# Performance work log

Measured on AMD Instinct MI355X. Metric: run time of the kernel, lower is better.

## Reference

```python
import jax, jax.numpy as jnp
import numpy as np

B, L, C, H, W = 1, 16, 32, 64, 64
HID = C // 2


def setup_inputs() -> dict:
    key = jax.random.key(0)
    ks = jax.random.split(key, 6)
    flows = jax.random.normal(ks[0], (B, L, 2, H, W), jnp.float32) * 0.05
    images = jax.random.normal(ks[1], (B, L, C, H, W), jnp.float32)
    w1 = jax.random.normal(ks[2], (HID, 2 * C), jnp.float32) * 0.05
    b1 = jax.random.normal(ks[3], (HID,), jnp.float32) * 0.05
    w2 = jax.random.normal(ks[4], (2, HID), jnp.float32) * 0.05
    b2 = jax.random.normal(ks[5], (2,), jnp.float32) * 0.01
    decay_log = jnp.asarray(-2.0, jnp.float32)
    return dict(flows=flows, images=images, decay_log=decay_log,
                w1=w1, b1=b1, w2=w2, b2=b2)


def _bilinear_sample(img, grid):
    # img: [C,H,W]; grid: [H,W,2] with (x,y) in [-1,1]; matches torch
    # grid_sample(mode='bilinear', padding_mode='zeros', align_corners=False)
    Cv, Hv, Wv = img.shape
    gx, gy = grid[..., 0], grid[..., 1]
    ix = ((gx + 1.0) * Wv - 1.0) * 0.5
    iy = ((gy + 1.0) * Hv - 1.0) * 0.5
    ix0 = jnp.floor(ix)
    iy0 = jnp.floor(iy)
    ix1, iy1 = ix0 + 1.0, iy0 + 1.0
    wx1 = ix - ix0
    wy1 = iy - iy0
    wx0 = 1.0 - wx1
    wy0 = 1.0 - wy1

    def corner(xi, yi, w):
        valid = (xi >= 0) & (xi < Wv) & (yi >= 0) & (yi < Hv)
        xc = jnp.clip(xi, 0, Wv - 1).astype(jnp.int32)
        yc = jnp.clip(yi, 0, Hv - 1).astype(jnp.int32)
        v = img[:, yc, xc]  # [C,H,W]
        return v * (w * valid.astype(img.dtype))[None]

    return (corner(ix0, iy0, wx0 * wy0) + corner(ix1, iy0, wx1 * wy0) +
            corner(ix0, iy1, wx0 * wy1) + corner(ix1, iy1, wx1 * wy1))


def _forward(flows, images, decay_log, w1, b1, w2, b2):
    Bv, Lv, Cv, Hv, Wv = images.shape
    cum = jnp.cumsum(flows, axis=1)                      # [B,L,2,H,W]
    rel = cum[:, :, None] - cum[:, None, :]              # [B,Lt,Lk,2,H,W]
    # residual 1x1 conv stack on concat(img_t, img_k)
    img_t = jnp.broadcast_to(images[:, :, None], (Bv, Lv, Lv, Cv, Hv, Wv))
    img_k = jnp.broadcast_to(images[:, None, :], (Bv, Lv, Lv, Cv, Hv, Wv))
    feat = jnp.concatenate([img_t, img_k], axis=3)       # [B,Lt,Lk,2C,H,W]
    h = jax.nn.relu(jnp.einsum('btkchw,oc->btkohw', feat, w1)
                    + b1[None, None, None, :, None, None])
    res = (jnp.einsum('btkohw,po->btkphw', h, w2)
           + b2[None, None, None, :, None, None])        # [B,Lt,Lk,2,H,W]
    rel = rel + res
    # base grid: pixel centers in [-1,1] (align_corners=False convention)
    gy = jnp.linspace(-1.0 + 1.0 / Hv, 1.0 - 1.0 / Hv, Hv, dtype=images.dtype)
    gx = jnp.linspace(-1.0 + 1.0 / Wv, 1.0 - 1.0 / Wv, Wv, dtype=images.dtype)
    base = jnp.stack(jnp.meshgrid(gx, gy, indexing='xy'), axis=-1)  # [H,W,2]
    grid = base + jnp.moveaxis(rel, 3, -1)               # [B,Lt,Lk,H,W,2]
    wrapped_x = jnp.mod(grid[..., 0] + 1.0, 2.0) - 1.0   # wrap x into [-1,1)
    grid = jnp.stack([wrapped_x, grid[..., 1]], axis=-1)
    # sample images[b,k] at grid[b,t,k] for all (t,k) pairs
    samp = jax.vmap(                                      # over batch
        jax.vmap(                                         # over t (grid only)
            jax.vmap(_bilinear_sample, (0, 0)),           # over k
            (None, 0)),
        (0, 0))(images, grid)                             # [B,Lt,Lk,C,H,W]
    # causal decay weights: exp(-exp(decay_log)*(t-k)) for k<=t, else 0
    tk = jnp.arange(Lv)[:, None] - jnp.arange(Lv)[None, :]
    wts = jnp.where(tk >= 0,
                    jnp.exp(-jnp.exp(decay_log) * tk.astype(images.dtype)),
                    jnp.zeros((), images.dtype))
    return jnp.einsum('btkchw,tk->btchw', samp, wts)


def reference(flows, images, decay_log, w1, b1, w2, b2):
    return _forward(flows, images, decay_log, w1, b1, w2, b2)
```

## Files before the change

kernel.cpp:

```cpp
#include <hip/hip_runtime.h>

#define LL 16
#define CC 32
#define HIDN 16
#define HH 64
#define WW 64
#define HW 4096
#define NCHUNK 40

#define CUM_OFF  0
#define U_OFF    (LL * 2 * HW)
#define V_OFF    (U_OFF + LL * HIDN * HW)
#define IMGC_OFF (V_OFF + LL * HIDN * HW)
#define A_OFF    (IMGC_OFF + LL * CC * HW / 2)

__device__ const int T_SORT[NCHUNK] = {
    0,1,2,3,4,5,6,7,8,9,10,11,12,13,14,15,
    4,5,6,7,8,9,10,11,12,13,14,15,
    8,9,10,11,12,13,14,15,
    12,13,14,15 };
__device__ const int KC_SORT[NCHUNK] = {
    0,0,0,0,0,0,0,0,0,0,0,0,0,0,0,0,
    1,1,1,1,1,1,1,1,1,1,1,1,
    2,2,2,2,2,2,2,2,
    3,3,3,3 };
__device__ const int SEG[4]  = {0, 16, 28, 36};
__device__ const int TMIN[4] = {0, 4, 8, 12};

__device__ inline unsigned short f2bf(float f) {
    unsigned u = __float_as_uint(f);
    unsigned r = (u + 0x7fffu + ((u >> 16) & 1u)) >> 16;
    return (unsigned short)r;
}
__device__ inline float bflo(unsigned u) { return __uint_as_float(u << 16); }
__device__ inline float bfhi(unsigned u) { return __uint_as_float(u & 0xffff0000u); }

__global__ __launch_bounds__(256) void cumsum_kernel(const float* __restrict__ flows,
                                                     float* __restrict__ cum) {
    int idx = blockIdx.x * 256 + threadIdx.x;
    float acc = 0.0f;
#pragma unroll
    for (int l = 0; l < LL; ++l) {
        acc += flows[l * 2 * HW + idx];
        cum[l * 2 * HW + idx] = acc;
    }
}

__global__ __launch_bounds__(256) void prep_kernel(const float* __restrict__ images,
                                                   const float* __restrict__ w1,
                                                   const float* __restrict__ b1,
                                                   float* __restrict__ ws) {
    __shared__ float w1s[HIDN * 2 * CC];
    const int tid = threadIdx.x;
    ((float4*)w1s)[tid] = ((const float4*)w1)[tid];
    __syncthreads();

    const int l  = blockIdx.y;
    const int px = blockIdx.x * 256 + tid;
    const float* img = images + (size_t)l * CC * HW;

    float x[CC];
#pragma unroll
    for (int c = 0; c < CC; ++c) x[c] = img[c * HW + px];

    float u[HIDN], v[HIDN];
#pragma unroll
    for (int o = 0; o < HIDN; ++o) { u[o] = 0.0f; v[o] = b1[o]; }
#pragma unroll
    for (int c = 0; c < CC; ++c) {
#pragma unroll
        for (int o = 0; o < HIDN; ++o) {
            u[o] = fmaf(w1s[o * 64 + c],      x[c], u[o]);
            v[o] = fmaf(w1s[o * 64 + CC + c], x[c], v[o]);
        }
    }

    float* Up = ws + U_OFF + (size_t)l * HIDN * HW + px;
    float* Vp = ws + V_OFF + (size_t)l * HIDN * HW + px;
#pragma unroll
    for (int o = 0; o < HIDN; ++o) {
        Up[o * HW] = u[o];
        Vp[o * HW] = v[o];
    }

    uint4* img4 = (uint4*)(ws + IMGC_OFF);
#pragma unroll
    for (int cg = 0; cg < 4; ++cg) {
        const int c0 = cg * 8;
        unsigned d[4];
#pragma unroll
        for (int q = 0; q < 4; ++q)
            d[q] = (unsigned)f2bf(x[c0 + 2 * q]) | ((unsigned)f2bf(x[c0 + 2 * q + 1]) << 16);
        img4[((size_t)(l * 4 + cg)) * HW + px] = make_uint4(d[0], d[1], d[2], d[3]);
    }
}

__global__ __launch_bounds__(256, 2) void sample_kernel(const float* __restrict__ ws_in,
                                                        float* __restrict__ ws_out,
                                                        const float* __restrict__ w2,
                                                        const float* __restrict__ b2,
                                                        const float* __restrict__ decay_log) {
    __shared__ float  w2s[2 * HIDN];
    __shared__ float  b2s2[2];
    __shared__ float2 dls[4][64];

    const int tid = threadIdx.x;
    if (tid < 2 * HIDN) w2s[tid] = w2[tid];
    if (tid < 2)        b2s2[tid] = b2[tid];
    __syncthreads();

    const int hwb = blockIdx.x;
    const int s   = (hwb & 7) * 320 + (hwb >> 3);
    const int cid = s >> 6;
    const int strip = s & 63;
    const int t   = T_SORT[cid];
    const int k0  = KC_SORT[cid] * 4;

    const float* cum = ws_in + CUM_OFF;
    const float* Ub  = ws_in + U_OFF;
    const float* Vb  = ws_in + V_OFF;
    const uint4* img4 = (const uint4*)(ws_in + IMGC_OFF);

    {
        const int kk  = tid >> 6;
        const int lp  = tid & 63;
        const int px1 = strip * 64 + lp;
        const int k1  = k0 + kk;

        const float* up = Ub + (size_t)t  * HIDN * HW + px1;
        const float* vp = Vb + (size_t)k1 * HIDN * HW + px1;

        float res0 = b2s2[0], res1 = b2s2[1];
#pragma unroll
        for (int o = 0; o < HIDN; ++o) {
            float h = fmaxf(up[o * HW] + vp[o * HW], 0.0f);
            res0 = fmaf(w2s[o],        h, res0);
            res1 = fmaf(w2s[HIDN + o], h, res1);
        }

        float dx = (cum[(t * 2)     * HW + px1] - cum[(k1 * 2)     * HW + px1]) + res0;
        float dy = (cum[(t * 2 + 1) * HW + px1] - cum[(k1 * 2 + 1) * HW + px1]) + res1;
        dls[kk][lp] = make_float2(dx, dy);
    }
    __syncthreads();

    const int lane = tid & 63;
    const int cg   = tid >> 6;
    const int px   = strip * 64 + lane;

    const float lam = expf(decay_log[0]);
    const float bgx = (float)(2 * lane  + 1) * (1.0f / 64.0f) - 1.0f;
    const float bgy = (float)(2 * strip + 1) * (1.0f / 64.0f) - 1.0f;

    int   off[4][4];
    float cwt[4][4];
#pragma unroll
    for (int dk = 0; dk < 4; ++dk) {
        const int k = k0 + dk;
        const float wtd = (k <= t) ? expf(-lam * (float)(t - k)) : 0.0f;
        float2 d = dls[dk][lane];

        float gx = bgx + d.x;
        float gy = bgy + d.y;

        float xp = gx + 1.0f;
        xp = xp - floorf(xp * 0.5f) * 2.0f;
        float gxw = xp - 1.0f;

        float ix = ((gxw + 1.0f) * 64.0f - 1.0f) * 0.5f;
        float iy = ((gy  + 1.0f) * 64.0f - 1.0f) * 0.5f;

        float ix0f = floorf(ix), iy0f = floorf(iy);
        float fx1 = ix - ix0f, fy1 = iy - iy0f;
        float fx0 = 1.0f - fx1, fy0 = 1.0f - fy1;
        int ix0 = (int)ix0f, iy0 = (int)iy0f;
        int ix1 = ix0 + 1,   iy1 = iy0 + 1;

        int xi[4] = {ix0, ix1, ix0, ix1};
        int yi[4] = {iy0, iy0, iy1, iy1};
        float wwv[4] = {fx0 * fy0, fx1 * fy0, fx0 * fy1, fx1 * fy1};
#pragma unroll
        for (int j = 0; j < 4; ++j) {
            bool valid = (xi[j] >= 0) & (xi[j] < WW) & (yi[j] >= 0) & (yi[j] < HH);
            int xc = min(max(xi[j], 0), WW - 1);
            int yc = min(max(yi[j], 0), HH - 1);
            off[dk][j] = yc * WW + xc;
            cwt[dk][j] = valid ? wwv[j] * wtd : 0.0f;
        }
    }

    uint4 q[4][4];
#pragma unroll
    for (int dk = 0; dk < 4; ++dk) {
        const size_t pb = (size_t)((k0 + dk) * 4 + cg) * HW;
#pragma unroll
        for (int j = 0; j < 4; ++j)
            q[dk][j] = img4[pb + off[dk][j]];
    }

    float acc[8];
#pragma unroll
    for (int j = 0; j < 8; ++j) acc[j] = 0.0f;

#pragma unroll
    for (int dk = 0; dk < 4; ++dk) {
#pragma unroll
        for (int j = 0; j < 4; ++j) {
            const float wj = cwt[dk][j];
            const uint4 v = q[dk][j];
            acc[0] = fmaf(wj, bflo(v.x), acc[0]);
            acc[1] = fmaf(wj, bfhi(v.x), acc[1]);
            acc[2] = fmaf(wj, bflo(v.y), acc[2]);
            acc[3] = fmaf(wj, bfhi(v.y), acc[3]);
            acc[4] = fmaf(wj, bflo(v.z), acc[4]);
            acc[5] = fmaf(wj, bfhi(v.z), acc[5]);
            acc[6] = fmaf(wj, bflo(v.w), acc[6]);
            acc[7] = fmaf(wj, bfhi(v.w), acc[7]);
        }
    }

    float* Ap = ws_out + A_OFF + ((size_t)cid * CC + cg * 8) * HW + px;
#pragma unroll
    for (int j = 0; j < 8; ++j) Ap[j * HW] = acc[j];
}

__global__ __launch_bounds__(256) void reduce_kernel(const float* __restrict__ ws,
                                                     float* __restrict__ out) {
    const int gid = blockIdx.x * 256 + threadIdx.x;
    const int t   = gid >> 15;
    const int c   = (gid >> 10) & 31;
    const int px4 = gid & 1023;

    const float4* A4 = (const float4*)(ws + A_OFF);
    const int n = 1 + (t >= 4) + (t >= 8) + (t >= 12);

    float4 s = make_float4(0.0f, 0.0f, 0.0f, 0.0f);
    for (int kc = 0; kc < n; ++kc) {
        int cid = SEG[kc] + (t - TMIN[kc]);
        float4 a = A4[((size_t)cid * CC + c) * (HW / 4) + px4];
        s.x += a.x; s.y += a.y; s.z += a.z; s.w += a.w;
    }
    ((float4*)out)[gid] = s;
}

extern "C" void kernel_launch(void* const* d_in, const int* in_sizes, int n_in,
                              void* d_out, int out_size, void* d_ws, size_t ws_size,
                              hipStream_t stream) {
    const float* flows     = (const float*)d_in[0];
    const float* images    = (const float*)d_in[1];
    const float* decay_log = (const float*)d_in[2];
    const float* w1        = (const float*)d_in[3];
    const float* b1        = (const float*)d_in[4];
    const float* w2        = (const float*)d_in[5];
    const float* b2        = (const float*)d_in[6];
    float* out = (float*)d_out;
    float* ws  = (float*)d_ws;

    cumsum_kernel<<<dim3(2 * HW / 256), dim3(256), 0, stream>>>(flows, ws + CUM_OFF);

    prep_kernel<<<dim3(HW / 256, LL), dim3(256), 0, stream>>>(images, w1, b1, ws);

    sample_kernel<<<dim3(8 * 320), dim3(256), 0, stream>>>(ws, ws, w2, b2, decay_log);

    reduce_kernel<<<dim3(2048), dim3(256), 0, stream>>>(ws, out);
}
```

Measured before the change: 110.3 us.

## Fuse cumsum into prep kernel and replace reduce pass with atomic accumulation

The cumsum kernel becomes an extra row of blocks in the prep kernel, which removes one launch. The sample kernel now atomically adds its per-chunk partial sums straight into the zeroed output instead of writing them to a workspace that a separate reduce kernel then summed. This drops a launch and a full write-then-read of the partial-sum buffer. In exchange it adds a memset and up to four-way float atomic contention per output element, and the summation order is no longer deterministic.

```diff
diff --git a/kernel.cpp b/kernel.cpp
--- a/kernel.cpp
+++ b/kernel.cpp
@@ -12,7 +12,6 @@
 #define U_OFF    (LL * 2 * HW)
 #define V_OFF    (U_OFF + LL * HIDN * HW)
 #define IMGC_OFF (V_OFF + LL * HIDN * HW)
-#define A_OFF    (IMGC_OFF + LL * CC * HW / 2)
 
 __device__ const int T_SORT[NCHUNK] = {
     0,1,2,3,4,5,6,7,8,9,10,11,12,13,14,15,
@@ -24,8 +23,6 @@
     1,1,1,1,1,1,1,1,1,1,1,1,
     2,2,2,2,2,2,2,2,
     3,3,3,3 };
-__device__ const int SEG[4]  = {0, 16, 28, 36};
-__device__ const int TMIN[4] = {0, 4, 8, 12};
 
 __device__ inline unsigned short f2bf(float f) {
     unsigned u = __float_as_uint(f);
@@ -35,23 +32,28 @@
 __device__ inline float bflo(unsigned u) { return __uint_as_float(u << 16); }
 __device__ inline float bfhi(unsigned u) { return __uint_as_float(u & 0xffff0000u); }
 
-__global__ __launch_bounds__(256) void cumsum_kernel(const float* __restrict__ flows,
-                                                     float* __restrict__ cum) {
-    int idx = blockIdx.x * 256 + threadIdx.x;
-    float acc = 0.0f;
-#pragma unroll
-    for (int l = 0; l < LL; ++l) {
-        acc += flows[l * 2 * HW + idx];
-        cum[l * 2 * HW + idx] = acc;
-    }
-}
-
 __global__ __launch_bounds__(256) void prep_kernel(const float* __restrict__ images,
+                                                   const float* __restrict__ flows,
                                                    const float* __restrict__ w1,
                                                    const float* __restrict__ b1,
                                                    float* __restrict__ ws) {
+    const int tid = threadIdx.x;
+
+    if (blockIdx.y == LL) {
+        const int g = blockIdx.x * 256 + tid;
+        float* cum = ws + CUM_OFF;
+        float a0 = 0.0f, a1 = 0.0f;
+#pragma unroll
+        for (int l = 0; l < LL; ++l) {
+            a0 += flows[l * 2 * HW + g];
+            a1 += flows[l * 2 * HW + HW + g];
+            cum[l * 2 * HW + g]      = a0;
+            cum[l * 2 * HW + HW + g] = a1;
+        }
+        return;
+    }
+
     __shared__ float w1s[HIDN * 2 * CC];
-    const int tid = threadIdx.x;
     ((float4*)w1s)[tid] = ((const float4*)w1)[tid];
     __syncthreads();
 
@@ -96,10 +98,10 @@
 }
 
 __global__ __launch_bounds__(256, 2) void sample_kernel(const float* __restrict__ ws_in,
-                                                        float* __restrict__ ws_out,
                                                         const float* __restrict__ w2,
                                                         const float* __restrict__ b2,
-                                                        const float* __restrict__ decay_log) {
+                                                        const float* __restrict__ decay_log,
+                                                        float* __restrict__ out) {
     __shared__ float  w2s[2 * HIDN];
     __shared__ float  b2s2[2];
     __shared__ float2 dls[4][64];
@@ -219,28 +221,9 @@
         }
     }
 
-    float* Ap = ws_out + A_OFF + ((size_t)cid * CC + cg * 8) * HW + px;
-#pragma unroll
-    for (int j = 0; j < 8; ++j) Ap[j * HW] = acc[j];
-}
-
-__global__ __launch_bounds__(256) void reduce_kernel(const float* __restrict__ ws,
-                                                     float* __restrict__ out) {
-    const int gid = blockIdx.x * 256 + threadIdx.x;
-    const int t   = gid >> 15;
-    const int c   = (gid >> 10) & 31;
-    const int px4 = gid & 1023;
-
-    const float4* A4 = (const float4*)(ws + A_OFF);
-    const int n = 1 + (t >= 4) + (t >= 8) + (t >= 12);
-
-    float4 s = make_float4(0.0f, 0.0f, 0.0f, 0.0f);
-    for (int kc = 0; kc < n; ++kc) {
-        int cid = SEG[kc] + (t - TMIN[kc]);
-        float4 a = A4[((size_t)cid * CC + c) * (HW / 4) + px4];
-        s.x += a.x; s.y += a.y; s.z += a.z; s.w += a.w;
-    }
-    ((float4*)out)[gid] = s;
+    float* Op = out + ((size_t)t * CC + cg * 8) * HW + px;
+#pragma unroll
+    for (int j = 0; j < 8; ++j) atomicAdd(Op + j * HW, acc[j]);
 }
 
 extern "C" void kernel_launch(void* const* d_in, const int* in_sizes, int n_in,
@@ -256,11 +239,11 @@
     float* out = (float*)d_out;
     float* ws  = (float*)d_ws;
 
-    cumsum_kernel<<<dim3(2 * HW / 256), dim3(256), 0, stream>>>(flows, ws + CUM_OFF);
-
-    prep_kernel<<<dim3(HW / 256, LL), dim3(256), 0, stream>>>(images, w1, b1, ws);
-
-    sample_kernel<<<dim3(8 * 320), dim3(256), 0, stream>>>(ws, ws, w2, b2, decay_log);
-
-    reduce_kernel<<<dim3(2048), dim3(256), 0, stream>>>(ws, out);
-}
+    hipMemsetAsync(d_out, 0, (size_t)out_size * sizeof(float), stream);
+
+    prep_kernel<<<dim3(HW / 256, LL + 1), dim3(256), 0, stream>>>(
+        images, flows, w1, b1, ws);
+
+    sample_kernel<<<dim3(8 * 320), dim3(256), 0, stream>>>(
+        ws, w2, b2, decay_log, out);
+}
```

New measurement: 116.8 us. +5.8%, slower.
